# Kernel tuning notes

Measured on AMD Instinct MI355X. Metric: run time of the kernel, lower is better.

Reference implementation:

```python
import jax, jax.numpy as jnp
import numpy as np

EPS = 1e-5


def setup_inputs() -> dict:
    key = jax.random.key(0)
    ks = jax.random.split(key, 5)
    b, c, L = 2, 512, 1024
    x = jax.random.normal(ks[0], (b, c, L), dtype=jnp.float32)
    gamma = jnp.ones((c,), dtype=jnp.float32)
    beta = jnp.zeros((c,), dtype=jnp.float32)
    w_qkv = jax.random.normal(ks[1], (3 * c, c), dtype=jnp.float32) * (1.0 / np.sqrt(c))
    b_qkv = jax.random.normal(ks[2], (3 * c,), dtype=jnp.float32) * 0.02
    # NOTE: original zero-inits proj_out; we use random weights for a
    # non-degenerate correctness baseline (same math, different init values).
    w_proj = jax.random.normal(ks[3], (c, c), dtype=jnp.float32) * (1.0 / np.sqrt(c))
    b_proj = jnp.zeros((c,), dtype=jnp.float32)
    return {"x": x, "gamma": gamma, "beta": beta, "w_qkv": w_qkv,
            "b_qkv": b_qkv, "w_proj": w_proj, "b_proj": b_proj, "num_heads": 8}


def reference(x, gamma, beta, w_qkv, b_qkv, w_proj, b_proj, num_heads):
    b, c, L = x.shape
    nh = int(num_heads)
    hd = c // nh
    # BatchNorm1d, training mode: stats over (batch, length) per channel
    mean = jnp.mean(x, axis=(0, 2), keepdims=True)
    var = jnp.mean((x - mean) ** 2, axis=(0, 2), keepdims=True)  # biased var
    xn = (x - mean) * jax.lax.rsqrt(var + EPS)
    xn = xn * gamma[None, :, None] + beta[None, :, None]
    # 1x1 conv == matmul over channel axis: (b, 3c, L)
    qkv = jnp.einsum('oc,bcl->bol', w_qkv, xn) + b_qkv[None, :, None]
    # Faithful (quirky) layout: (b, 3*nh, hd, L) -> (b, hd, L, 3*nh)
    qkv = qkv.reshape(b, 3 * nh, hd, L).transpose(0, 2, 3, 1)
    q, k, v = jnp.split(qkv, 3, axis=-1)  # each (b, hd, L, nh)
    scale = (3 * nh) ** (-0.5)  # original scales by qkv's last dim before chunk
    # scores: (b, hd, T, T) -- 'heads' axis is hd due to the layout quirk
    w = jax.nn.softmax(jnp.einsum('bhtd,bhfd->bhtf', q * scale, k), axis=-1)
    a = jnp.einsum('bhtf,bhfd->bhtd', w, v)  # (b, hd, L, nh)
    h = a.transpose(0, 3, 1, 2).reshape(b, c, L)
    h = jnp.einsum('oc,bcl->bol', w_proj, h) + b_proj[None, :, None]
    return x + h
```

## Files before the change

kernel.cpp:

```cpp
#include <hip/hip_runtime.h>
#include <hip/hip_bf16.h>
#include <cstddef>
#include <cstdint>

#define B_ 2
#define C_ 512
#define L_ 1024
#define NH_ 8
#define HD_ 64
#define OC_ 1536

typedef short short8 __attribute__((ext_vector_type(8)));
typedef short short4v __attribute__((ext_vector_type(4)));
typedef float f32x4 __attribute__((ext_vector_type(4)));
typedef __fp16 f16x4 __attribute__((ext_vector_type(4)));
typedef __fp16 f16x2 __attribute__((ext_vector_type(2)));

#if defined(__has_builtin)
#if __has_builtin(__builtin_amdgcn_exp2f)
#define FEXP2(x) __builtin_amdgcn_exp2f(x)
#endif
#endif
#ifndef FEXP2
#define FEXP2(x) exp2f(x)
#endif

__device__ inline float bf_bits_to_f32(unsigned short u) {
  union { unsigned u32; float f; } c; c.u32 = ((unsigned)u) << 16; return c.f;
}
__device__ inline short f32_to_bf_bits(float f) {
  union { float f; unsigned u; } c; c.f = f;
  return (short)((c.u + 0x7FFFu + ((c.u >> 16) & 1u)) >> 16);
}

__device__ __forceinline__ void gl2lds16(const short* g, short* l) {
  __builtin_amdgcn_global_load_lds(
      (const __attribute__((address_space(1))) unsigned*)(const void*)g,
      (__attribute__((address_space(3))) unsigned*)(void*)l, 16, 0, 0);
}

__global__ __launch_bounds__(256) void prep_kernel(
    const float* __restrict__ x, const float* __restrict__ gamma,
    const float* __restrict__ beta, const float* __restrict__ w_qkv,
    const float* __restrict__ w_proj,
    float* __restrict__ s_out, float* __restrict__ t_out,
    short* __restrict__ wq16, short* __restrict__ wpp16)
{
  const int bid = blockIdx.x;
  const int tid = threadIdx.x;
  if (bid < 512) {
    const int ch = bid;
    const float4 v0 = *(const float4*)(x + (size_t)ch * L_ + tid * 4);
    const float4 v1 = *(const float4*)(x + (size_t)(C_ + ch) * L_ + tid * 4);
    float s1 = v0.x + v0.y + v0.z + v0.w + v1.x + v1.y + v1.z + v1.w;
    float s2 = v0.x*v0.x + v0.y*v0.y + v0.z*v0.z + v0.w*v0.w
             + v1.x*v1.x + v1.y*v1.y + v1.z*v1.z + v1.w*v1.w;
    #pragma unroll
    for (int off = 32; off > 0; off >>= 1) {
      s1 += __shfl_down(s1, off);
      s2 += __shfl_down(s2, off);
    }
    __shared__ float r1[4], r2[4];
    const int wid = tid >> 6, lane = tid & 63;
    if (lane == 0) { r1[wid] = s1; r2[wid] = s2; }
    __syncthreads();
    if (tid == 0) {
      const float S1 = r1[0] + r1[1] + r1[2] + r1[3];
      const float S2 = r2[0] + r2[1] + r2[2] + r2[3];
      const float invN = 1.f / (float)(B_ * L_);
      const float mean = S1 * invN;
      const float var  = S2 * invN - mean * mean;
      const float rstd = rsqrtf(var + 1e-5f);
      const float sc = gamma[ch] * rstd;
      s_out[ch] = sc;
      t_out[ch] = beta[ch] - mean * sc;
    }
  } else if (bid < 704) {
    const int base = (bid - 512) * 4096 + tid * 16;
    #pragma unroll
    for (int it = 0; it < 2; ++it) {
      const float4 a0 = *(const float4*)(w_qkv + base + it * 8);
      const float4 a1 = *(const float4*)(w_qkv + base + it * 8 + 4);
      short8 v;
      v[0] = f32_to_bf_bits(a0.x); v[1] = f32_to_bf_bits(a0.y);
      v[2] = f32_to_bf_bits(a0.z); v[3] = f32_to_bf_bits(a0.w);
      v[4] = f32_to_bf_bits(a1.x); v[5] = f32_to_bf_bits(a1.y);
      v[6] = f32_to_bf_bits(a1.z); v[7] = f32_to_bf_bits(a1.w);
      *(short8*)(wq16 + base + it * 8) = v;
    }
  } else {
    #pragma unroll
    for (int grp = 0; grp < 4; ++grp) {
      const int idx = (bid - 704) * 4096 + tid * 16 + grp * 4;
      const int o = idx >> 9, cp = idx & 511;
      short4v v;
      #pragma unroll
      for (int j = 0; j < 4; ++j) {
        const int c = ((cp + j) & 7) * 64 + ((cp + j) >> 3);
        v[j] = f32_to_bf_bits(w_proj[(size_t)o * C_ + c]);
      }
      *(short4v*)(wpp16 + (size_t)o * C_ + cp) = v;
    }
  }
}

__global__ __launch_bounds__(256) void xt_kernel(
    const float* __restrict__ x, const float* __restrict__ s,
    const float* __restrict__ t, short* __restrict__ xT)
{
  __shared__ float T[64][65];
  const int t0 = blockIdx.x * 64, c0 = blockIdx.y * 64, b = blockIdx.z;
  const int tid = threadIdx.x;
  const float* xp = x + (size_t)b * C_ * L_;
  #pragma unroll
  for (int it = 0; it < 4; ++it) {
    const int idx = it * 256 + tid;
    const int rr = idx >> 4, c4 = (idx & 15) * 4;
    const float4 v = *(const float4*)(xp + (size_t)(c0 + rr) * L_ + t0 + c4);
    const float sc = s[c0 + rr], tc = t[c0 + rr];
    T[rr][c4 + 0] = fmaf(v.x, sc, tc);
    T[rr][c4 + 1] = fmaf(v.y, sc, tc);
    T[rr][c4 + 2] = fmaf(v.z, sc, tc);
    T[rr][c4 + 3] = fmaf(v.w, sc, tc);
  }
  __syncthreads();
  #pragma unroll
  for (int it = 0; it < 4; ++it) {
    const int idx = it * 256 + tid;
    const int tt_ = idx >> 4, cc4 = (idx & 15) * 4;
    short4v o;
    #pragma unroll
    for (int j = 0; j < 4; ++j) o[j] = f32_to_bf_bits(T[cc4 + j][tt_]);
    *(short4v*)(xT + ((size_t)b * L_ + t0 + tt_) * C_ + c0 + cc4) = o;
  }
}

template <int MR, int NR, bool OUT_BF16>
__global__ __launch_bounds__(256) void gemm_bt16_kernel(
    const short* __restrict__ A, const short* __restrict__ B,
    const float* __restrict__ bias, const float* __restrict__ res,
    void* __restrict__ Cv, int M, int N, int K,
    size_t sB, size_t sC, size_t sR)
{
  constexpr int BM = MR * 32, BN = NR * 32;
  __shared__ short As[BM * 64];
  __shared__ short Bs[BN * 64];
  const int tid = threadIdx.x;
  const int l = tid & 63, w = tid >> 6;
  const int wr = w >> 1, wc = w & 1;
  const int ll = l & 15;
  const int n0 = blockIdx.x * BN, m0 = blockIdx.y * BM, bz = blockIdx.z;
  const short* Bg = B + (size_t)bz * sB;
  f32x4 acc[MR][NR] = {};

  for (int k0 = 0; k0 < K; k0 += 64) {
    #pragma unroll
    for (int it = 0; it < BM / 32; ++it) {
      const int row0 = w * (BM / 4) + it * 8;
      const int row = row0 + (l >> 3), sl = l & 7;
      gl2lds16(A + (size_t)(m0 + row) * K + k0 + ((sl ^ (row & 7)) * 8),
               As + row0 * 64);
    }
    #pragma unroll
    for (int it = 0; it < BN / 32; ++it) {
      const int row0 = w * (BN / 4) + it * 8;
      const int row = row0 + (l >> 3), sl = l & 7;
      gl2lds16(Bg + (size_t)(n0 + row) * K + k0 + ((sl ^ (row & 7)) * 8),
               Bs + row0 * 64);
    }
    __syncthreads();
    #pragma unroll
    for (int kk = 0; kk < 2; ++kk) {
      short8 af[MR], bfg[NR];
      const int sd = kk * 4 + (l >> 4);
      #pragma unroll
      for (int m = 0; m < MR; ++m) {
        const int ra = wr * MR * 16 + m * 16 + ll;
        af[m] = *(const short8*)(As + ra * 64 + (sd ^ (ra & 7)) * 8);
      }
      #pragma unroll
      for (int n = 0; n < NR; ++n) {
        const int rb = wc * NR * 16 + n * 16 + ll;
        bfg[n] = *(const short8*)(Bs + rb * 64 + (sd ^ (rb & 7)) * 8);
      }
      #pragma unroll
      for (int m = 0; m < MR; ++m)
        #pragma unroll
        for (int n = 0; n < NR; ++n)
          acc[m][n] = __builtin_amdgcn_mfma_f32_16x16x32_bf16(
              af[m], bfg[n], acc[m][n], 0, 0, 0);
    }
    __syncthreads();
  }

  const int rg4 = (l >> 4) * 4;
  __hip_bfloat16* Cb = (__hip_bfloat16*)Cv + (size_t)bz * sC;
  float* Cf = (float*)Cv + (size_t)bz * sC;
  const float* Rp = res + (size_t)bz * sR;
  #pragma unroll
  for (int m = 0; m < MR; ++m) {
    #pragma unroll
    for (int reg = 0; reg < 4; ++reg) {
      const int gm = m0 + wr * MR * 16 + m * 16 + rg4 + reg;
      const float bv = bias[gm];
      #pragma unroll
      for (int n = 0; n < NR; ++n) {
        const int gn = n0 + wc * NR * 16 + n * 16 + ll;
        float v = acc[m][n][reg] + bv;
        if (OUT_BF16) {
          Cb[(size_t)gm * N + gn] = __hip_bfloat16_raw{(unsigned short)f32_to_bf_bits(v)};
        } else {
          v += Rp[(size_t)gm * N + gn];
          Cf[(size_t)gm * N + gn] = v;
        }
      }
    }
  }
}

__global__ __launch_bounds__(256, 4) void attn_kernel(
    const __hip_bfloat16* __restrict__ qkv, short* __restrict__ hT)
{
  __shared__ __fp16 Klds[1024 * 8];
  __shared__ __fp16 Vlds[9 * 1032];

  const int tq = blockIdx.x, d = blockIdx.y, b = blockIdx.z;
  const int tid = threadIdx.x;
  const int w = tid >> 6, l = tid & 63;
  const int hi = l >> 4, ll = l & 15;
  const int t0 = tq * 128 + w * 32;
  const short* base = (const short*)qkv + (size_t)b * OC_ * L_;
  short* KldsS = (short*)Klds;
  short* VldsS = (short*)Vlds;

  #pragma unroll
  for (int it = 0; it < 4; ++it) {
    const int f = it * 256 + tid;
    unsigned u[4];
    #pragma unroll
    for (int e = 0; e < 4; ++e) {
      const f16x2 p = __builtin_amdgcn_cvt_pkrtz(
          bf_bits_to_f32((unsigned short)base[(size_t)((8 + 2*e)   * HD_ + d) * L_ + f]),
          bf_bits_to_f32((unsigned short)base[(size_t)((8 + 2*e+1) * HD_ + d) * L_ + f]));
      u[e] = __builtin_bit_cast(unsigned, p);
    }
    uint4 uu; uu.x = u[0]; uu.y = u[1]; uu.z = u[2]; uu.w = u[3];
    *(uint4*)(KldsS + f * 8) = uu;
  }
  #pragma unroll
  for (int it = 0; it < 4; ++it) {
    const int i = it * 256 + tid;
    const int g = i >> 7, fs = i & 127;
    const short8 v = *(const short8*)(
        base + (size_t)((16 + g) * HD_ + d) * L_ + fs * 8);
    unsigned u[4];
    #pragma unroll
    for (int e = 0; e < 4; ++e) {
      const f16x2 p = __builtin_amdgcn_cvt_pkrtz(
          bf_bits_to_f32((unsigned short)v[2 * e]),
          bf_bits_to_f32((unsigned short)v[2 * e + 1]));
      u[e] = __builtin_bit_cast(unsigned, p);
    }
    uint4 uu; uu.x = u[0]; uu.y = u[1]; uu.z = u[2]; uu.w = u[3];
    *(uint4*)(VldsS + g * 1032 + fs * 8) = uu;
  }
  {
    uint2 ones; ones.x = 0x3C003C00u; ones.y = 0x3C003C00u;
    *(uint2*)(VldsS + 8 * 1032 + tid * 4) = ones;
  }

  f16x4 bQ[2] = {};
  if (l < 32) {
    const int g0 = 4 * hi;
    #pragma unroll
    for (int tt = 0; tt < 2; ++tt) {
      const int t = t0 + tt * 16 + ll;
      float q[4];
      #pragma unroll
      for (int j = 0; j < 4; ++j)
        q[j] = bf_bits_to_f32(
                   (unsigned short)base[(size_t)((g0 + j) * HD_ + d) * L_ + t]) *
               0.29448889f;
      const f16x2 a = __builtin_amdgcn_cvt_pkrtz(q[0], q[1]);
      const f16x2 bb = __builtin_amdgcn_cvt_pkrtz(q[2], q[3]);
      union { f16x4 v; uint2 u; } m;
      m.u.x = __builtin_bit_cast(unsigned, a);
      m.u.y = __builtin_bit_cast(unsigned, bb);
      bQ[tt] = m.v;
    }
  }

  __syncthreads();

  const int vrow = (ll < 9) ? ll : 8;
  const f32x4 z4 = {0.f, 0.f, 0.f, 0.f};
  f32x4 accO[2] = {};
  const __fp16* akB = Klds + ll * 8 + 4 * (hi & 1);
  const __fp16* avB = Vlds + vrow * 1032 + 4 * hi;

  #pragma unroll
  for (int c = 0; c < 8; ++c) {
    #pragma unroll
    for (int ft = 0; ft < 8; ++ft) {
      const f16x4 ak = *(const f16x4*)(akB + c * 1024 + ft * 128);
      const f16x4 av = *(const f16x4*)(avB + c * 128 + ft * 16);
      #pragma unroll
      for (int tt = 0; tt < 2; ++tt) {
        const f32x4 s = __builtin_amdgcn_mfma_f32_16x16x16f16(
            ak, bQ[tt], z4, 0, 0, 0);
        const f16x2 p0 = __builtin_amdgcn_cvt_pkrtz(FEXP2(s[0]), FEXP2(s[1]));
        const f16x2 p1 = __builtin_amdgcn_cvt_pkrtz(FEXP2(s[2]), FEXP2(s[3]));
        union { f16x4 v; uint2 u; } bp;
        bp.u.x = __builtin_bit_cast(unsigned, p0);
        bp.u.y = __builtin_bit_cast(unsigned, p1);
        accO[tt] = __builtin_amdgcn_mfma_f32_16x16x16f16(av, bp.v, accO[tt], 0, 0, 0);
      }
    }
  }

  __syncthreads();
  short* Olds = KldsS;
  #pragma unroll
  for (int nt = 0; nt < 2; ++nt) {
    const float sum = __shfl(accO[nt][0], 32 + ll);
    const float inv = 1.f / sum;
    if (hi < 2) {
      const int tl = w * 32 + nt * 16 + ll;
      #pragma unroll
      for (int reg = 0; reg < 4; ++reg)
        Olds[tl * 8 + hi * 4 + reg] = f32_to_bf_bits(accO[nt][reg] * inv);
    }
  }
  __syncthreads();
  if (tid < 128) {
    const short8 ov = *(const short8*)(Olds + tid * 8);
    *(short8*)(hT + ((size_t)b * L_ + tq * 128 + tid) * C_ + d * 8) = ov;
  }
}

extern "C" void kernel_launch(void* const* d_in, const int* in_sizes, int n_in,
                              void* d_out, int out_size, void* d_ws, size_t ws_size,
                              hipStream_t stream) {
  (void)in_sizes; (void)n_in; (void)out_size; (void)ws_size;
  const float* x      = (const float*)d_in[0];
  const float* gamma  = (const float*)d_in[1];
  const float* beta   = (const float*)d_in[2];
  const float* w_qkv  = (const float*)d_in[3];
  const float* b_qkv  = (const float*)d_in[4];
  const float* w_proj = (const float*)d_in[5];
  const float* b_proj = (const float*)d_in[6];
  float* out = (float*)d_out;
  char* wsb = (char*)d_ws;

  float* s_buf = (float*)(wsb + 0);
  float* t_buf = (float*)(wsb + 2048);
  short* wq16  = (short*)(wsb + 4096);
  short* wpp16 = (short*)(wsb + 4096 + 1572864);
  short* xT    = (short*)(wsb + 4096 + 2097152);
  short* qkv   = (short*)(wsb + 4096 + 4194304);
  short* hT    = (short*)(wsb + 4096 + 10485760);

  hipLaunchKernelGGL(prep_kernel, dim3(768), dim3(256), 0, stream,
                     x, gamma, beta, w_qkv, w_proj, s_buf, t_buf, wq16, wpp16);
  hipLaunchKernelGGL(xt_kernel, dim3(L_ / 64, C_ / 64, B_), dim3(256), 0, stream,
                     x, s_buf, t_buf, xT);
  hipLaunchKernelGGL((gemm_bt16_kernel<2, 2, true>),
                     dim3(L_ / 64, OC_ / 64, B_), dim3(256), 0, stream,
                     wq16, xT, b_qkv, (const float*)nullptr, (void*)qkv,
                     OC_, L_, C_, (size_t)L_ * C_, (size_t)OC_ * L_, (size_t)0);
  hipLaunchKernelGGL(attn_kernel, dim3(8, HD_, B_), dim3(256), 0, stream,
                     (const __hip_bfloat16*)qkv, hT);
  hipLaunchKernelGGL((gemm_bt16_kernel<1, 2, false>),
                     dim3(L_ / 64, C_ / 32, B_), dim3(256), 0, stream,
                     wpp16, hT, b_proj, x, (void*)out,
                     C_, L_, C_, (size_t)L_ * C_, (size_t)C_ * L_, (size_t)C_ * L_);
}
```

Before: 48.94 us.

## Fuse BatchNorm stats into transpose kernel with redundant per-block statistics

Merges the BN-statistics pass and the normalize-transpose kernel into one launch. Each of the 256 transpose blocks recomputes mean and variance for its own 64 channels over the full batch and length, so the intermediate scale/shift buffers and one kernel boundary disappear. The cost is redundant reads of x: each channel's statistics are recomputed by 32 blocks (16 time tiles times 2 batches), and the per-wave serial loop over 16 channels lengthens the critical path of those blocks.

```diff
diff --git a/kernel.cpp b/kernel.cpp
--- a/kernel.cpp
+++ b/kernel.cpp
@@ -39,44 +39,74 @@
       (__attribute__((address_space(3))) unsigned*)(void*)l, 16, 0, 0);
 }
 
-__global__ __launch_bounds__(256) void prep_kernel(
+__global__ __launch_bounds__(256) void fused_pre_kernel(
     const float* __restrict__ x, const float* __restrict__ gamma,
     const float* __restrict__ beta, const float* __restrict__ w_qkv,
-    const float* __restrict__ w_proj,
-    float* __restrict__ s_out, float* __restrict__ t_out,
+    const float* __restrict__ w_proj, short* __restrict__ xT,
     short* __restrict__ wq16, short* __restrict__ wpp16)
 {
   const int bid = blockIdx.x;
   const int tid = threadIdx.x;
-  if (bid < 512) {
-    const int ch = bid;
-    const float4 v0 = *(const float4*)(x + (size_t)ch * L_ + tid * 4);
-    const float4 v1 = *(const float4*)(x + (size_t)(C_ + ch) * L_ + tid * 4);
-    float s1 = v0.x + v0.y + v0.z + v0.w + v1.x + v1.y + v1.z + v1.w;
-    float s2 = v0.x*v0.x + v0.y*v0.y + v0.z*v0.z + v0.w*v0.w
-             + v1.x*v1.x + v1.y*v1.y + v1.z*v1.z + v1.w*v1.w;
-    #pragma unroll
-    for (int off = 32; off > 0; off >>= 1) {
-      s1 += __shfl_down(s1, off);
-      s2 += __shfl_down(s2, off);
-    }
-    __shared__ float r1[4], r2[4];
-    const int wid = tid >> 6, lane = tid & 63;
-    if (lane == 0) { r1[wid] = s1; r2[wid] = s2; }
+  if (bid < 256) {
+    __shared__ float T[64][65];
+    __shared__ float sS[64], tS[64];
+    const int t0 = (bid & 15) * 64, c0 = ((bid >> 4) & 7) * 64, b = bid >> 7;
+    const int w = tid >> 6, l = tid & 63;
+
+    for (int i = 0; i < 16; ++i) {
+      const int ch = c0 + w * 16 + i;
+      float s1 = 0.f, s2 = 0.f;
+      #pragma unroll
+      for (int bb = 0; bb < 2; ++bb) {
+        const float* p = x + (size_t)(bb * C_ + ch) * L_;
+        #pragma unroll
+        for (int q = 0; q < 4; ++q) {
+          const float4 v = *(const float4*)(p + q * 256 + l * 4);
+          s1 += (v.x + v.y) + (v.z + v.w);
+          s2 += (v.x*v.x + v.y*v.y) + (v.z*v.z + v.w*v.w);
+        }
+      }
+      #pragma unroll
+      for (int off = 32; off > 0; off >>= 1) {
+        s1 += __shfl_down(s1, off);
+        s2 += __shfl_down(s2, off);
+      }
+      if (l == 0) {
+        const float invN = 1.f / (float)(B_ * L_);
+        const float mean = s1 * invN;
+        const float var  = s2 * invN - mean * mean;
+        const float rstd = rsqrtf(var + 1e-5f);
+        const float sc = gamma[ch] * rstd;
+        sS[w * 16 + i] = sc;
+        tS[w * 16 + i] = beta[ch] - mean * sc;
+      }
+    }
     __syncthreads();
-    if (tid == 0) {
-      const float S1 = r1[0] + r1[1] + r1[2] + r1[3];
-      const float S2 = r2[0] + r2[1] + r2[2] + r2[3];
-      const float invN = 1.f / (float)(B_ * L_);
-      const float mean = S1 * invN;
-      const float var  = S2 * invN - mean * mean;
-      const float rstd = rsqrtf(var + 1e-5f);
-      const float sc = gamma[ch] * rstd;
-      s_out[ch] = sc;
-      t_out[ch] = beta[ch] - mean * sc;
-    }
-  } else if (bid < 704) {
-    const int base = (bid - 512) * 4096 + tid * 16;
+
+    const float* xp = x + (size_t)b * C_ * L_;
+    #pragma unroll
+    for (int it = 0; it < 4; ++it) {
+      const int idx = it * 256 + tid;
+      const int rr = idx >> 4, c4 = (idx & 15) * 4;
+      const float4 v = *(const float4*)(xp + (size_t)(c0 + rr) * L_ + t0 + c4);
+      const float sc = sS[rr], tc = tS[rr];
+      T[rr][c4 + 0] = fmaf(v.x, sc, tc);
+      T[rr][c4 + 1] = fmaf(v.y, sc, tc);
+      T[rr][c4 + 2] = fmaf(v.z, sc, tc);
+      T[rr][c4 + 3] = fmaf(v.w, sc, tc);
+    }
+    __syncthreads();
+    #pragma unroll
+    for (int it = 0; it < 4; ++it) {
+      const int idx = it * 256 + tid;
+      const int tt_ = idx >> 4, cc4 = (idx & 15) * 4;
+      short4v o;
+      #pragma unroll
+      for (int j = 0; j < 4; ++j) o[j] = f32_to_bf_bits(T[cc4 + j][tt_]);
+      *(short4v*)(xT + ((size_t)b * L_ + t0 + tt_) * C_ + c0 + cc4) = o;
+    }
+  } else if (bid < 448) {
+    const int base = (bid - 256) * 4096 + tid * 16;
     #pragma unroll
     for (int it = 0; it < 2; ++it) {
       const float4 a0 = *(const float4*)(w_qkv + base + it * 8);
@@ -91,7 +121,7 @@
   } else {
     #pragma unroll
     for (int grp = 0; grp < 4; ++grp) {
-      const int idx = (bid - 704) * 4096 + tid * 16 + grp * 4;
+      const int idx = (bid - 448) * 4096 + tid * 16 + grp * 4;
       const int o = idx >> 9, cp = idx & 511;
       short4v v;
       #pragma unroll
@@ -101,37 +131,6 @@
       }
       *(short4v*)(wpp16 + (size_t)o * C_ + cp) = v;
     }
-  }
-}
-
-__global__ __launch_bounds__(256) void xt_kernel(
-    const float* __restrict__ x, const float* __restrict__ s,
-    const float* __restrict__ t, short* __restrict__ xT)
-{
-  __shared__ float T[64][65];
-  const int t0 = blockIdx.x * 64, c0 = blockIdx.y * 64, b = blockIdx.z;
-  const int tid = threadIdx.x;
-  const float* xp = x + (size_t)b * C_ * L_;
-  #pragma unroll
-  for (int it = 0; it < 4; ++it) {
-    const int idx = it * 256 + tid;
-    const int rr = idx >> 4, c4 = (idx & 15) * 4;
-    const float4 v = *(const float4*)(xp + (size_t)(c0 + rr) * L_ + t0 + c4);
-    const float sc = s[c0 + rr], tc = t[c0 + rr];
-    T[rr][c4 + 0] = fmaf(v.x, sc, tc);
-    T[rr][c4 + 1] = fmaf(v.y, sc, tc);
-    T[rr][c4 + 2] = fmaf(v.z, sc, tc);
-    T[rr][c4 + 3] = fmaf(v.w, sc, tc);
-  }
-  __syncthreads();
-  #pragma unroll
-  for (int it = 0; it < 4; ++it) {
-    const int idx = it * 256 + tid;
-    const int tt_ = idx >> 4, cc4 = (idx & 15) * 4;
-    short4v o;
-    #pragma unroll
-    for (int j = 0; j < 4; ++j) o[j] = f32_to_bf_bits(T[cc4 + j][tt_]);
-    *(short4v*)(xT + ((size_t)b * L_ + t0 + tt_) * C_ + c0 + cc4) = o;
   }
 }
 
@@ -352,18 +351,14 @@
   float* out = (float*)d_out;
   char* wsb = (char*)d_ws;
 
-  float* s_buf = (float*)(wsb + 0);
-  float* t_buf = (float*)(wsb + 2048);
   short* wq16  = (short*)(wsb + 4096);
   short* wpp16 = (short*)(wsb + 4096 + 1572864);
   short* xT    = (short*)(wsb + 4096 + 2097152);
   short* qkv   = (short*)(wsb + 4096 + 4194304);
   short* hT    = (short*)(wsb + 4096 + 10485760);
 
-  hipLaunchKernelGGL(prep_kernel, dim3(768), dim3(256), 0, stream,
-                     x, gamma, beta, w_qkv, w_proj, s_buf, t_buf, wq16, wpp16);
-  hipLaunchKernelGGL(xt_kernel, dim3(L_ / 64, C_ / 64, B_), dim3(256), 0, stream,
-                     x, s_buf, t_buf, xT);
+  hipLaunchKernelGGL(fused_pre_kernel, dim3(512), dim3(256), 0, stream,
+                     x, gamma, beta, w_qkv, w_proj, xT, wq16, wpp16);
   hipLaunchKernelGGL((gemm_bt16_kernel<2, 2, true>),
                      dim3(L_ / 64, OC_ / 64, B_), dim3(256), 0, stream,
                      wq16, xT, b_qkv, (const float*)nullptr, (void*)qkv,
```

New measurement: 59.61 us. 1.22x slower.
